# Kernel tuning notes

Hardware: AMD Instinct MI355X
Metric: run time of the kernel (lower is better)

The kernel has to match this reference:

```python
import jax, jax.numpy as jnp
import numpy as np

D_MODEL = 192; N_HEAD = 6; N_LEVELS = 3; N_POINTS = 4; D_HEAD = D_MODEL // N_HEAD
W_IMG = 1024.0; H_IMG = 1024.0
STRIDES = (8.0, 16.0, 32.0)
SIGMAS = (4.0, 2.0, 1.0)
N_FREQ = 8


def fourier_pe(coords):
    # coords [..., 2] -> [..., 4*N_FREQ]
    freqs = 2.0 ** jnp.arange(N_FREQ, dtype=jnp.float32)
    x = coords[..., 0:1] * freqs * (2.0 * jnp.pi)
    y = coords[..., 1:2] * freqs * (2.0 * jnp.pi)
    return jnp.concatenate([jnp.sin(x), jnp.cos(x), jnp.sin(y), jnp.cos(y)], axis=-1)


def bilinear_sample(feat, pts):
    # feat [B, H, d_h, Hl, Wl]; pts [B, K, R, H, M, 2] (x, y) in feature-pixel coords
    # zero padding outside the map (torch grid_sample padding_mode='zeros', align_corners=True)
    B, Hh, dh, Hl, Wl = feat.shape
    featf = feat.transpose(0, 1, 3, 4, 2).reshape(B, Hh, Hl * Wl, dh)
    x = pts[..., 0]; y = pts[..., 1]
    x0 = jnp.floor(x); y0 = jnp.floor(y)
    wx1 = x - x0; wy1 = y - y0
    wx0 = 1.0 - wx1; wy0 = 1.0 - wy1
    x0i = x0.astype(jnp.int32); y0i = y0.astype(jnp.int32)
    b_idx = jnp.arange(B)[:, None, None, None, None]
    h_idx = jnp.arange(Hh)[None, None, None, :, None]

    def gather(xi, yi):
        valid = (xi >= 0) & (xi < Wl) & (yi >= 0) & (yi < Hl)
        lin = jnp.clip(yi, 0, Hl - 1) * Wl + jnp.clip(xi, 0, Wl - 1)
        v = featf[b_idx, h_idx, lin]  # [B,K,R,H,M,dh]
        return v * valid[..., None].astype(feat.dtype)

    out = (gather(x0i, y0i) * (wx0 * wy0)[..., None]
           + gather(x0i + 1, y0i) * (wx1 * wy0)[..., None]
           + gather(x0i, y0i + 1) * (wx0 * wy1)[..., None]
           + gather(x0i + 1, y0i + 1) * (wx1 * wy1)[..., None])
    return out


def layernorm(x, g, b, eps=1e-5):
    mu = jnp.mean(x, axis=-1, keepdims=True)
    var = jnp.var(x, axis=-1, keepdims=True)
    return (x - mu) * jax.lax.rsqrt(var + eps) * g + b


def setup_inputs():
    key = jax.random.key(0)
    ks = jax.random.split(key, 16)
    B, K, R = 2, 256, 32
    H4 = W4 = 32
    s = 0.02
    inp = {}
    inp['h'] = jax.random.normal(ks[0], (B, K, D_MODEL), jnp.float32)
    inp['top_indices'] = jax.random.randint(ks[1], (B, K, R), 0, H4 * W4)
    inp['query_coords'] = jax.random.uniform(ks[2], (B, K, 2), jnp.float32) * jnp.array([W_IMG, H_IMG], jnp.float32)
    inp['g'] = jax.random.normal(ks[3], (B, H4 * W4, D_MODEL), jnp.float32)
    inp['L2_proj'] = jax.random.normal(ks[4], (B, D_MODEL, 128, 128), jnp.float32)
    inp['L3_proj'] = jax.random.normal(ks[5], (B, D_MODEL, 64, 64), jnp.float32)
    inp['L4_proj'] = jax.random.normal(ks[6], (B, D_MODEL, 32, 32), jnp.float32)
    inp['w_u_w'] = jax.random.normal(ks[7], (D_MODEL, 2 * D_MODEL + 32), jnp.float32) * s
    inp['w_u_b'] = jnp.zeros((D_MODEL,), jnp.float32)
    inp['ln_u_g'] = jnp.ones((D_MODEL,), jnp.float32)
    inp['ln_u_b'] = jnp.zeros((D_MODEL,), jnp.float32)
    inp['w_delta_w'] = jax.random.normal(ks[8], (N_HEAD * N_LEVELS * N_POINTS * 2, D_MODEL), jnp.float32) * s
    inp['w_delta_b'] = jax.random.normal(ks[9], (N_HEAD * N_LEVELS * N_POINTS * 2,), jnp.float32) * s
    inp['w_a_w'] = jax.random.normal(ks[10], (N_HEAD * N_LEVELS * N_POINTS, D_MODEL), jnp.float32) * s
    inp['w_a_b'] = jnp.zeros((N_HEAD * N_LEVELS * N_POINTS,), jnp.float32)
    inp['w_o_w'] = jax.random.normal(ks[11], (D_MODEL, D_MODEL), jnp.float32) * s
    inp['w_o_b'] = jnp.zeros((D_MODEL,), jnp.float32)
    inp['e_deform'] = jax.random.normal(ks[12], (1, 1, 1, D_MODEL), jnp.float32) * s
    return inp


def reference(h, top_indices, query_coords, g, L2_proj, L3_proj, L4_proj,
              w_u_w, w_u_b, ln_u_g, ln_u_b, w_delta_w, w_delta_b,
              w_a_w, w_a_b, w_o_w, w_o_b, e_deform):
    B, K, d = h.shape
    R = top_indices.shape[2]
    H, d_h, L, M = N_HEAD, D_HEAD, N_LEVELS, N_POINTS
    H4, W4 = L4_proj.shape[2], L4_proj.shape[3]

    # anchor pixel coordinates from L4 indices
    stride_4 = STRIDES[2]
    anchor_x = (top_indices % W4).astype(jnp.float32)
    anchor_y = (top_indices // W4).astype(jnp.float32)
    anchor_px = jnp.stack([anchor_x * stride_4 + stride_4 / 2,
                           anchor_y * stride_4 + stride_4 / 2], axis=-1)  # [B,K,R,2]

    # gather global tokens at anchors
    b_idx = jnp.arange(B)[:, None, None]
    g_r = g[b_idx, top_indices]  # [B,K,R,d]

    # relative position encoding
    delta_p = anchor_px - query_coords[:, :, None, :]
    delta_p_norm = delta_p / jnp.array([W_IMG, H_IMG], jnp.float32)
    phi = fourier_pe(delta_p_norm)  # [B,K,R,32]

    h_exp = jnp.broadcast_to(h[:, :, None, :], (B, K, R, d))
    u_input = jnp.concatenate([h_exp, g_r, phi], axis=-1)  # [B,K,R,2d+32]
    u_r = layernorm(jax.nn.gelu(jnp.einsum('bkrc,dc->bkrd', u_input, w_u_w) + w_u_b,
                                approximate=False), ln_u_g, ln_u_b)

    raw_offsets = (jnp.einsum('bkrd,od->bkro', u_r, w_delta_w) + w_delta_b
                   ).reshape(B, K, R, H, L, M, 2)
    logits = (jnp.einsum('bkrd,od->bkro', u_r, w_a_w) + w_a_b).reshape(B, K, R, H, L * M)
    weights = jax.nn.softmax(logits, axis=-1).reshape(B, K, R, H, L, M)

    proj_maps = [L2_proj, L3_proj, L4_proj]
    h_r = jnp.zeros((B, K, R, H, d_h), h.dtype)
    for l in range(L):
        feat = proj_maps[l]
        Hl, Wl = feat.shape[2], feat.shape[3]
        feat = feat.reshape(B, H, d_h, Hl, Wl)
        anchor_feat = anchor_px / STRIDES[l]  # [B,K,R,2]
        off = jnp.tanh(raw_offsets[:, :, :, :, l]) * SIGMAS[l]  # [B,K,R,H,M,2]
        pts = anchor_feat[:, :, :, None, None, :] + off  # [B,K,R,H,M,2]
        sampled = bilinear_sample(feat, pts)  # [B,K,R,H,M,d_h]
        h_r = h_r + jnp.einsum('bkrhmc,bkrhm->bkrhc', sampled, weights[:, :, :, :, l])

    h_r = h_r.reshape(B, K, R, d)
    deform_tokens = jnp.einsum('bkrd,od->bkro', h_r, w_o_w) + w_o_b + e_deform
    return deform_tokens
```

## Files before the change

### kernel.cpp

```cpp
#include <hip/hip_runtime.h>
#include <hip/hip_bf16.h>

typedef __hip_bfloat16 bf16;
typedef __attribute__((ext_vector_type(8))) short s8b;
typedef __attribute__((ext_vector_type(4))) float f32x4;

__device__ __forceinline__ float us2f(unsigned short u) {
  union { unsigned int i; float f; } v; v.i = ((unsigned int)u) << 16; return v.f;
}
__device__ __forceinline__ float ldf(const void* p, int i, bool f32m) {
  return f32m ? ((const float*)p)[i] : us2f(((const unsigned short*)p)[i]);
}
__device__ __forceinline__ bool sniff_f32(const void* ln_g_ones) {
  return ((const unsigned int*)ln_g_ones)[0] == 0x3F800000u;
}
__device__ __forceinline__ short f2bs(float x) {
  bf16 v = __float2bfloat16(x); short s; __builtin_memcpy(&s, &v, 2); return s;
}
__device__ __forceinline__ s8b cvt8(const float* p) {
  s8b r;
  #pragma unroll
  for (int j = 0; j < 8; ++j) r[j] = f2bs(p[j]);
  return r;
}

__global__ __launch_bounds__(256) void prep_all(
    const void* __restrict__ L2, const void* __restrict__ L3,
    const void* __restrict__ L4,
    const void* __restrict__ wu,  const void* __restrict__ wub,
    const void* __restrict__ lng, const void* __restrict__ lnb,
    const void* __restrict__ wd,  const void* __restrict__ wdb,
    const void* __restrict__ wa,  const void* __restrict__ wab,
    const void* __restrict__ wo,  const void* __restrict__ wob,
    const void* __restrict__ ed,  const void* __restrict__ h,
    bf16* __restrict__ f2, bf16* __restrict__ f3, bf16* __restrict__ f4,
    bf16* __restrict__ wb1, bf16* __restrict__ wb2, bf16* __restrict__ wb3,
    float* __restrict__ ln_g, float* __restrict__ ln_b,
    float* __restrict__ wda_b, float* __restrict__ wo_be,
    float* __restrict__ hdotAll, const int useT)
{
  __shared__ float tile[64][65];
  const bool f32m = sniff_f32(lng);
  const int t = threadIdx.x;
  int bid = blockIdx.x;

  if (bid < 2016) {
    if (!useT) return;
    const void* src; bf16* dst; int HW, spt;
    if (bid < 1536)      { src = L2; dst = f2; HW = 16384; spt = 256; }
    else if (bid < 1920) { bid -= 1536; src = L3; dst = f3; HW = 4096; spt = 64; }
    else                 { bid -= 1920; src = L4; dst = f4; HW = 1024; spt = 16; }
    int ct = bid % 3; bid /= 3;
    int st = bid % spt; int b = bid / spt;
    int sp0 = st * 64, ch0 = ct * 64;
    int sp4 = t & 15, cy0 = t >> 4;
    if (f32m) {
      #pragma unroll
      for (int i = 0; i < 4; ++i) {
        int cy = cy0 + 16 * i;
        const float* s4 = (const float*)src + (size_t)(b * 192 + ch0 + cy) * HW + sp0 + 4 * sp4;
        float4 v = *(const float4*)s4;
        tile[4 * sp4 + 0][cy] = v.x;
        tile[4 * sp4 + 1][cy] = v.y;
        tile[4 * sp4 + 2][cy] = v.z;
        tile[4 * sp4 + 3][cy] = v.w;
      }
    } else {
      #pragma unroll
      for (int i = 0; i < 4; ++i) {
        int cy = cy0 + 16 * i;
        #pragma unroll
        for (int k = 0; k < 4; ++k)
          tile[4 * sp4 + k][cy] =
              ldf(src, (b * 192 + ch0 + cy) * HW + sp0 + 4 * sp4 + k, f32m);
      }
    }
    __syncthreads();
    #pragma unroll
    for (int i = 0; i < 2; ++i) {
      int u = t + 256 * i;
      int sp = u >> 3, c8 = u & 7;
      const float* row = &tile[sp][c8 * 8];
      s8b pk;
      #pragma unroll
      for (int j = 0; j < 8; ++j) pk[j] = f2bs(row[j]);
      *(s8b*)&dst[(size_t)(b * HW + sp0 + sp) * 192 + ch0 + c8 * 8] = pk;
    }
  } else if (bid < 2528) {
    int i0 = (bid - 2016) * 256 + t;
    const int stride = 512 * 256;
    for (int i = i0; i < 192 * 224; i += stride) {
      int d = i / 224, cc = i - d * 224;
      int ks = cc >> 5, r32 = cc & 31, q = r32 >> 3, j = r32 & 7;
      int lane = q * 16 + (d & 15), nt = d >> 4;
      wb1[((ks * 12 + nt) * 64 + lane) * 8 + j] =
          __float2bfloat16(ldf(wu, d * 416 + 192 + cc, f32m));
    }
    for (int i = i0; i < 144 * 192; i += stride) {
      int o = i / 192, c = i - o * 192;
      int ks = c >> 5, r32 = c & 31, q = r32 >> 3, j = r32 & 7;
      int lane = q * 16 + (o & 15), nt = o >> 4;
      wb2[((ks * 14 + nt) * 64 + lane) * 8 + j] = __float2bfloat16(ldf(wd, i, f32m));
    }
    for (int i = i0; i < 72 * 192; i += stride) {
      int o = 144 + i / 192, c = i % 192;
      int ks = c >> 5, r32 = c & 31, q = r32 >> 3, j = r32 & 7;
      int lane = q * 16 + (o & 15), nt = o >> 4;
      wb2[((ks * 14 + nt) * 64 + lane) * 8 + j] = __float2bfloat16(ldf(wa, i, f32m));
    }
    for (int i = i0; i < 192 * 192; i += stride) {
      int o = i / 192, dK = i - o * 192;
      int ks = dK >> 5, r32 = dK & 31, q = r32 >> 3, j = r32 & 7;
      int lane = q * 16 + (o & 15), nt = o >> 4;
      wb3[((ks * 12 + nt) * 64 + lane) * 8 + j] = __float2bfloat16(ldf(wo, i, f32m));
    }
    if (i0 < 192) {
      ln_g[i0]  = ldf(lng, i0, f32m);
      ln_b[i0]  = ldf(lnb, i0, f32m);
      wo_be[i0] = ldf(wob, i0, f32m) + ldf(ed, i0, f32m);
    }
    if (i0 < 216) wda_b[i0] = (i0 < 144) ? ldf(wdb, i0, f32m) : ldf(wab, i0 - 144, f32m);
  } else {
    int bk = bid - 2528;
    int lane = t & 63, wv = t >> 6;
    float hv0 = ldf(h, bk * 192 + lane, f32m);
    float hv1 = ldf(h, bk * 192 + 64 + lane, f32m);
    float hv2 = ldf(h, bk * 192 + 128 + lane, f32m);
    for (int r = 0; r < 48; ++r) {
      int d = wv + 4 * r;
      float p = hv0 * ldf(wu, d * 416 + lane, f32m);
      p = fmaf(hv1, ldf(wu, d * 416 + 64 + lane, f32m), p);
      p = fmaf(hv2, ldf(wu, d * 416 + 128 + lane, f32m), p);
      #pragma unroll
      for (int off = 32; off >= 1; off >>= 1) p += __shfl_xor(p, off);
      if (lane == 0) hdotAll[bk * 192 + d] = p + ldf(wub, d, f32m);
    }
  }
}

__global__ __launch_bounds__(384) void fused_k(
    const int* __restrict__ topi, const void* __restrict__ qc,
    const void* __restrict__ g, const float* __restrict__ hdotAll,
    const bf16* __restrict__ wb1, const bf16* __restrict__ wb2,
    const bf16* __restrict__ wb3,
    const float* __restrict__ ln_g, const float* __restrict__ ln_b,
    const float* __restrict__ wda_b, const float* __restrict__ wo_be,
    const void* __restrict__ lng_raw,
    const bf16* __restrict__ f2, const bf16* __restrict__ f3,
    const bf16* __restrict__ f4,
    const void* __restrict__ L2, const void* __restrict__ L3,
    const void* __restrict__ L4, const int useT,
    float* __restrict__ out)
{
  __shared__ float uni[16 * 216];
  __shared__ float u_sh[16][196];
  __shared__ float anch[16][2];
  __shared__ int   idx_sh[16];
  __shared__ float qxy[2];
  __shared__ float stats[16][2];
  short* gpb = (short*)uni;
  float* ol  = uni;

  const bool f32m = sniff_f32(lng_raw);
  const int t = threadIdx.x;
  const int lane = t & 63, wv = t >> 6;
  const int m16 = lane & 15, quad = lane >> 4;
  const int bk = blockIdx.x >> 1;
  const int b = bk >> 8;
  const int tok0 = blockIdx.x * 16;

  if (t < 2) qxy[t] = ldf(qc, bk * 2 + t, f32m);
  if (t < 16) {
    int idx = topi[tok0 + t];
    idx_sh[t] = idx;
    anch[t][0] = (float)(idx & 31) * 32.f + 16.f;
    anch[t][1] = (float)(idx >> 5) * 32.f + 16.f;
  }
  __syncthreads();

  if (f32m) {
    #pragma unroll
    for (int i = 0; i < 2; ++i) {
      int u = t + 384 * i;
      int r = u / 48, q4 = u - r * 48;
      const float* s4 = (const float*)g + (size_t)(b * 1024 + idx_sh[r]) * 192 + 4 * q4;
      float4 v = *(const float4*)s4;
      short pk[4] = { f2bs(v.x), f2bs(v.y), f2bs(v.z), f2bs(v.w) };
      *(uint2*)&gpb[r * 232 + 4 * q4] = *(const uint2*)pk;
    }
  } else {
    for (int u = t; u < 16 * 192; u += 384) {
      int r = u / 192, j = u - r * 192;
      gpb[r * 232 + j] = f2bs(ldf(g, (b * 1024 + idx_sh[r]) * 192 + j, f32m));
    }
  }
  for (int u = t; u < 16 * 32; u += 384) {
    int r = u >> 5, j = u & 31;
    float dn = (((j & 16) ? (anch[r][1] - qxy[1]) : (anch[r][0] - qxy[0]))) * (1.f / 1024.f);
    float a = dn * (float)(1 << (j & 7)) * 6.283185307179586f;
    gpb[r * 232 + 192 + j] = f2bs((j & 8) ? cosf(a) : sinf(a));
  }
  __syncthreads();

  {
    s8b afr[7];
    #pragma unroll
    for (int ks = 0; ks < 7; ++ks)
      afr[ks] = *(const s8b*)&gpb[m16 * 232 + ks * 32 + quad * 8];
    const s8b* wbv = (const s8b*)wb1;
    #pragma unroll
    for (int nt = 0; nt < 2; ++nt) {
      int ntile = wv * 2 + nt;
      float bias = hdotAll[bk * 192 + ntile * 16 + m16];
      f32x4 acc = { bias, bias, bias, bias };
      #pragma unroll
      for (int ks = 0; ks < 7; ++ks) {
        s8b bfr = wbv[(ks * 12 + ntile) * 64 + lane];
        acc = __builtin_amdgcn_mfma_f32_16x16x32_bf16(afr[ks], bfr, acc, 0, 0, 0);
      }
      #pragma unroll
      for (int reg = 0; reg < 4; ++reg) {
        float x = acc[reg];
        u_sh[quad * 4 + reg][ntile * 16 + m16] =
            0.5f * x * (1.f + erff(x * 0.70710678118654752f));
      }
    }
  }
  __syncthreads();

  if (t < 256) {
    int r = t >> 4, i = t & 15;
    float s = 0.f, s2 = 0.f;
    #pragma unroll
    for (int j = 0; j < 12; ++j) { float v = u_sh[r][i * 12 + j]; s += v; s2 += v * v; }
    #pragma unroll
    for (int d = 8; d >= 1; d >>= 1) { s += __shfl_xor(s, d); s2 += __shfl_xor(s2, d); }
    if (i == 0) {
      float mu = s * (1.f / 192.f);
      float var = s2 * (1.f / 192.f) - mu * mu;
      stats[r][0] = mu; stats[r][1] = rsqrtf(var + 1e-5f);
    }
  }
  __syncthreads();
  for (int u = t; u < 16 * 192; u += 384) {
    int r = u / 192, dd = u - r * 192;
    u_sh[r][dd] = (u_sh[r][dd] - stats[r][0]) * stats[r][1] * ln_g[dd] + ln_b[dd];
  }
  __syncthreads();

  {
    s8b afr[6];
    #pragma unroll
    for (int ks = 0; ks < 6; ++ks)
      afr[ks] = cvt8(&u_sh[m16][ks * 32 + quad * 8]);
    const s8b* wbv = (const s8b*)wb2;
    #pragma unroll
    for (int i = 0; i < 3; ++i) {
      int ntile = wv + 6 * i;
      if (ntile < 14) {
        int o0 = ntile * 16 + m16;
        float bias = (o0 < 216) ? wda_b[o0] : 0.f;
        f32x4 acc = { bias, bias, bias, bias };
        #pragma unroll
        for (int ks = 0; ks < 6; ++ks) {
          s8b bfr = wbv[(ks * 14 + ntile) * 64 + lane];
          acc = __builtin_amdgcn_mfma_f32_16x16x32_bf16(afr[ks], bfr, acc, 0, 0, 0);
        }
        if (o0 < 216) {
          #pragma unroll
          for (int reg = 0; reg < 4; ++reg)
            ol[(quad * 4 + reg) * 216 + o0] = acc[reg];
        }
      }
    }
  }
  __syncthreads();

  for (int u = t; u < 16 * 144; u += 384) {
    int r = u / 144, o = u - r * 144;
    int l = (o >> 3) % 3;
    ol[r * 216 + o] = tanhf(ol[r * 216 + o]) * (float)(4 >> l);
  }
  if (t < 96) {
    int r = t / 6, hh = t - r * 6;
    float* lg = &ol[r * 216 + 144 + hh * 12];
    float mx = lg[0];
    for (int i = 1; i < 12; ++i) mx = fmaxf(mx, lg[i]);
    float s = 0.f;
    for (int i = 0; i < 12; ++i) { float e = expf(lg[i] - mx); lg[i] = e; s += e; }
    float inv = 1.f / s;
    for (int i = 0; i < 12; ++i) lg[i] *= inv;
  }
  __syncthreads();

  {
    int tl = t / 24, c8 = t - tl * 24;
    int hc0 = c8 * 8;
    int hh = hc0 >> 5;
    float ax = anch[tl][0], ay = anch[tl][1];
    const float* olp = &ol[tl * 216];
    float acc[8];
    #pragma unroll
    for (int j = 0; j < 8; ++j) acc[j] = 0.f;

    const bf16* ftsT[3] = { f2, f3, f4 };
    const void* ftsO[3] = { L2, L3, L4 };
    #pragma unroll
    for (int l = 0; l < 3; ++l) {
      const int Hl = 128 >> l;
      const bf16* ftT = ftsT[l];
      const void* ftO = ftsO[l];
      float inv_s = 1.f / (float)(8 << l);
      float bx = ax * inv_s, by = ay * inv_s;
      #pragma unroll
      for (int m = 0; m < 4; ++m) {
        int ob = ((hh * 3 + l) * 4 + m) * 2;
        float px = bx + olp[ob];
        float py = by + olp[ob + 1];
        float fx = floorf(px), fy = floorf(py);
        int x0 = (int)fx, y0 = (int)fy;
        float wx1 = px - fx, wy1 = py - fy;
        float wx0 = 1.f - wx1, wy0 = 1.f - wy1;
        int xc0 = min(max(x0, 0), Hl - 1),   xc1 = min(max(x0 + 1, 0), Hl - 1);
        int yc0 = min(max(y0, 0), Hl - 1),   yc1 = min(max(y0 + 1, 0), Hl - 1);
        bool vx0 = (x0 >= 0) & (x0 < Hl),    vx1 = (x0 + 1 >= 0) & (x0 + 1 < Hl);
        bool vy0 = (y0 >= 0) & (y0 < Hl),    vy1 = (y0 + 1 >= 0) & (y0 + 1 < Hl);
        float aw = olp[144 + hh * 12 + l * 4 + m];
        float w00 = (vx0 && vy0) ? wx0 * wy0 * aw : 0.f;
        float w01 = (vx1 && vy0) ? wx1 * wy0 * aw : 0.f;
        float w10 = (vx0 && vy1) ? wx0 * wy1 * aw : 0.f;
        float w11 = (vx1 && vy1) ? wx1 * wy1 * aw : 0.f;
        if (useT) {
          const s8b* p00 = (const s8b*)&ftT[((b * Hl + yc0) * Hl + xc0) * 192 + hc0];
          const s8b* p01 = (const s8b*)&ftT[((b * Hl + yc0) * Hl + xc1) * 192 + hc0];
          const s8b* p10 = (const s8b*)&ftT[((b * Hl + yc1) * Hl + xc0) * 192 + hc0];
          const s8b* p11 = (const s8b*)&ftT[((b * Hl + yc1) * Hl + xc1) * 192 + hc0];
          s8b v00 = *p00, v01 = *p01, v10 = *p10, v11 = *p11;
          #pragma unroll
          for (int j = 0; j < 8; ++j) {
            float s = us2f((unsigned short)v00[j]) * w00
                    + us2f((unsigned short)v01[j]) * w01
                    + us2f((unsigned short)v10[j]) * w10
                    + us2f((unsigned short)v11[j]) * w11;
            acc[j] += s;
          }
        } else {
          #pragma unroll
          for (int j = 0; j < 8; ++j) {
            int ch = hc0 + j;
            float s = ldf(ftO, ((b * 192 + ch) * Hl + yc0) * Hl + xc0, f32m) * w00
                    + ldf(ftO, ((b * 192 + ch) * Hl + yc0) * Hl + xc1, f32m) * w01
                    + ldf(ftO, ((b * 192 + ch) * Hl + yc1) * Hl + xc0, f32m) * w10
                    + ldf(ftO, ((b * 192 + ch) * Hl + yc1) * Hl + xc1, f32m) * w11;
            acc[j] += s;
          }
        }
      }
    }
    #pragma unroll
    for (int j = 0; j < 8; ++j) u_sh[tl][hc0 + j] = acc[j];
  }
  __syncthreads();

  {
    s8b afr[6];
    #pragma unroll
    for (int ks = 0; ks < 6; ++ks)
      afr[ks] = cvt8(&u_sh[m16][ks * 32 + quad * 8]);
    const s8b* wbv = (const s8b*)wb3;
    #pragma unroll
    for (int nt = 0; nt < 2; ++nt) {
      int ntile = wv * 2 + nt;
      int n = ntile * 16 + m16;
      float bias = wo_be[n];
      f32x4 acc = { bias, bias, bias, bias };
      #pragma unroll
      for (int ks = 0; ks < 6; ++ks) {
        s8b bfr = wbv[(ks * 12 + ntile) * 64 + lane];
        acc = __builtin_amdgcn_mfma_f32_16x16x32_bf16(afr[ks], bfr, acc, 0, 0, 0);
      }
      #pragma unroll
      for (int reg = 0; reg < 4; ++reg)
        out[(long long)(tok0 + quad * 4 + reg) * 192 + n] = acc[reg];
    }
  }
}

extern "C" void kernel_launch(void* const* d_in, const int* in_sizes, int n_in,
                              void* d_out, int out_size, void* d_ws, size_t ws_size,
                              hipStream_t stream)
{
  const void* h    = d_in[0];
  const int*  topi = (const int*)d_in[1];
  const void* qc   = d_in[2];
  const void* g    = d_in[3];
  const void* L2p  = d_in[4];
  const void* L3p  = d_in[5];
  const void* L4p  = d_in[6];
  const void* wu   = d_in[7];
  const void* wub  = d_in[8];
  const void* lng  = d_in[9];
  const void* lnb  = d_in[10];
  const void* wd   = d_in[11];
  const void* wdb  = d_in[12];
  const void* wa   = d_in[13];
  const void* wab  = d_in[14];
  const void* wo   = d_in[15];
  const void* wob  = d_in[16];
  const void* ed   = d_in[17];
  float* outp = (float*)d_out;

  char* ws = (char*)d_ws;
  size_t off = 0;
  auto take = [&](size_t bytes) {
    char* p = ws + off;
    off += (bytes + 255) & ~(size_t)255;
    return p;
  };
  bf16*  wb1     = (bf16*)take(7ULL * 12 * 64 * 8 * 2);
  bf16*  wb2     = (bf16*)take(6ULL * 14 * 64 * 8 * 2);
  bf16*  wb3     = (bf16*)take(6ULL * 12 * 64 * 8 * 2);
  float* lngf    = (float*)take(192 * 4);
  float* lnbf    = (float*)take(192 * 4);
  float* wda_b   = (float*)take(216 * 4);
  float* wo_be   = (float*)take(192 * 4);
  float* hdotAll = (float*)take(512ULL * 192 * 4);
  size_t feat_bytes = (2ULL * 192 * 128 * 128 + 2ULL * 192 * 64 * 64 + 2ULL * 192 * 32 * 32) * 2 + 1024;
  int useT = (ws_size >= off + feat_bytes) ? 1 : 0;
  bf16* f2 = (bf16*)take(useT ? 2ULL * 192 * 128 * 128 * 2 : 0);
  bf16* f3 = (bf16*)take(useT ? 2ULL * 192 * 64 * 64 * 2 : 0);
  bf16* f4 = (bf16*)take(useT ? 2ULL * 192 * 32 * 32 * 2 : 0);
  (void)in_sizes; (void)n_in; (void)out_size;

  hipLaunchKernelGGL(prep_all, dim3(3040), dim3(256), 0, stream,
                     L2p, L3p, L4p, wu, wub, lng, lnb, wd, wdb, wa, wab,
                     wo, wob, ed, h, f2, f3, f4, wb1, wb2, wb3,
                     lngf, lnbf, wda_b, wo_be, hdotAll, useT);
  hipLaunchKernelGGL(fused_k, dim3(1024), dim3(384), 0, stream,
                     topi, qc, g, hdotAll, wb1, wb2, wb3,
                     lngf, lnbf, wda_b, wo_be, lng,
                     f2, f3, f4, L2p, L3p, L4p, useT, outp);
}
```

Before: 192.2 us.

## Replace LDS-tiled feature transpose with direct per-thread gather and packed bf16 FMA

The feature-map NCHW→NHWC bf16 conversion in the prep kernel drops its 64x64 shared-memory tile transpose. Each thread now reads 8 channel values directly with strided loads and writes one 16-byte packed vector, and the grid grows to match. The sampling loop in the fused kernel also unpacks bf16 pairs from 32-bit words and accumulates into 2-wide float vectors, to allow packed FMA. The direct gather gives up coalesced reads in the transpose, since the 8 loads per thread hit addresses HW apart, which may raise global memory traffic in exchange for removing the LDS round trip and the barrier.

```diff
diff --git a/kernel.cpp b/kernel.cpp
--- a/kernel.cpp
+++ b/kernel.cpp
@@ -4,6 +4,7 @@
 typedef __hip_bfloat16 bf16;
 typedef __attribute__((ext_vector_type(8))) short s8b;
 typedef __attribute__((ext_vector_type(4))) float f32x4;
+typedef __attribute__((ext_vector_type(2))) float v2f;
 
 __device__ __forceinline__ float us2f(unsigned short u) {
   union { unsigned int i; float f; } v; v.i = ((unsigned int)u) << 16; return v.f;
@@ -22,6 +23,11 @@
   #pragma unroll
   for (int j = 0; j < 8; ++j) r[j] = f2bs(p[j]);
   return r;
+}
+__device__ __forceinline__ v2f bf2x(unsigned int u) {
+  union { unsigned int i; float f; } lo, hi;
+  lo.i = u << 16; hi.i = u & 0xffff0000u;
+  v2f r; r.x = lo.f; r.y = hi.f; return r;
 }
 
 __global__ __launch_bounds__(256) void prep_all(
@@ -39,55 +45,25 @@
     float* __restrict__ wda_b, float* __restrict__ wo_be,
     float* __restrict__ hdotAll, const int useT)
 {
-  __shared__ float tile[64][65];
   const bool f32m = sniff_f32(lng);
   const int t = threadIdx.x;
   int bid = blockIdx.x;
 
-  if (bid < 2016) {
+  if (bid < 4032) {
     if (!useT) return;
-    const void* src; bf16* dst; int HW, spt;
-    if (bid < 1536)      { src = L2; dst = f2; HW = 16384; spt = 256; }
-    else if (bid < 1920) { bid -= 1536; src = L3; dst = f3; HW = 4096; spt = 64; }
-    else                 { bid -= 1920; src = L4; dst = f4; HW = 1024; spt = 16; }
-    int ct = bid % 3; bid /= 3;
-    int st = bid % spt; int b = bid / spt;
-    int sp0 = st * 64, ch0 = ct * 64;
-    int sp4 = t & 15, cy0 = t >> 4;
-    if (f32m) {
-      #pragma unroll
-      for (int i = 0; i < 4; ++i) {
-        int cy = cy0 + 16 * i;
-        const float* s4 = (const float*)src + (size_t)(b * 192 + ch0 + cy) * HW + sp0 + 4 * sp4;
-        float4 v = *(const float4*)s4;
-        tile[4 * sp4 + 0][cy] = v.x;
-        tile[4 * sp4 + 1][cy] = v.y;
-        tile[4 * sp4 + 2][cy] = v.z;
-        tile[4 * sp4 + 3][cy] = v.w;
-      }
-    } else {
-      #pragma unroll
-      for (int i = 0; i < 4; ++i) {
-        int cy = cy0 + 16 * i;
-        #pragma unroll
-        for (int k = 0; k < 4; ++k)
-          tile[4 * sp4 + k][cy] =
-              ldf(src, (b * 192 + ch0 + cy) * HW + sp0 + 4 * sp4 + k, f32m);
-      }
-    }
-    __syncthreads();
-    #pragma unroll
-    for (int i = 0; i < 2; ++i) {
-      int u = t + 256 * i;
-      int sp = u >> 3, c8 = u & 7;
-      const float* row = &tile[sp][c8 * 8];
-      s8b pk;
-      #pragma unroll
-      for (int j = 0; j < 8; ++j) pk[j] = f2bs(row[j]);
-      *(s8b*)&dst[(size_t)(b * HW + sp0 + sp) * 192 + ch0 + c8 * 8] = pk;
-    }
-  } else if (bid < 2528) {
-    int i0 = (bid - 2016) * 256 + t;
+    int u = bid * 256 + t;
+    int c8 = u % 24, gpix = u / 24;
+    const void* src; bf16* dst; int HW, b, sp;
+    if (gpix < 32768)      { src = L2; dst = f2; HW = 16384; b = gpix >> 14; sp = gpix & 16383; }
+    else if (gpix < 40960) { gpix -= 32768; src = L3; dst = f3; HW = 4096; b = gpix >> 12; sp = gpix & 4095; }
+    else                   { gpix -= 40960; src = L4; dst = f4; HW = 1024; b = gpix >> 10; sp = gpix & 1023; }
+    s8b pk;
+    #pragma unroll
+    for (int j = 0; j < 8; ++j)
+      pk[j] = f2bs(ldf(src, (b * 192 + c8 * 8 + j) * HW + sp, f32m));
+    *(s8b*)&dst[(size_t)(b * HW + sp) * 192 + c8 * 8] = pk;
+  } else if (bid < 4544) {
+    int i0 = (bid - 4032) * 256 + t;
     const int stride = 512 * 256;
     for (int i = i0; i < 192 * 224; i += stride) {
       int d = i / 224, cc = i - d * 224;
@@ -121,7 +97,7 @@
     }
     if (i0 < 216) wda_b[i0] = (i0 < 144) ? ldf(wdb, i0, f32m) : ldf(wab, i0 - 144, f32m);
   } else {
-    int bk = bid - 2528;
+    int bk = bid - 4544;
     int lane = t & 63, wv = t >> 6;
     float hv0 = ldf(h, bk * 192 + lane, f32m);
     float hv1 = ldf(h, bk * 192 + 64 + lane, f32m);
@@ -299,9 +275,9 @@
     int hh = hc0 >> 5;
     float ax = anch[tl][0], ay = anch[tl][1];
     const float* olp = &ol[tl * 216];
-    float acc[8];
-    #pragma unroll
-    for (int j = 0; j < 8; ++j) acc[j] = 0.f;
+    v2f acc2[4];
+    #pragma unroll
+    for (int p = 0; p < 4; ++p) { acc2[p].x = 0.f; acc2[p].y = 0.f; }
 
     const bf16* ftsT[3] = { f2, f3, f4 };
     const void* ftsO[3] = { L2, L3, L4 };
@@ -331,34 +307,42 @@
         float w10 = (vx0 && vy1) ? wx0 * wy1 * aw : 0.f;
         float w11 = (vx1 && vy1) ? wx1 * wy1 * aw : 0.f;
         if (useT) {
-          const s8b* p00 = (const s8b*)&ftT[((b * Hl + yc0) * Hl + xc0) * 192 + hc0];
-          const s8b* p01 = (const s8b*)&ftT[((b * Hl + yc0) * Hl + xc1) * 192 + hc0];
-          const s8b* p10 = (const s8b*)&ftT[((b * Hl + yc1) * Hl + xc0) * 192 + hc0];
-          const s8b* p11 = (const s8b*)&ftT[((b * Hl + yc1) * Hl + xc1) * 192 + hc0];
-          s8b v00 = *p00, v01 = *p01, v10 = *p10, v11 = *p11;
+          uint4 u00 = *(const uint4*)&ftT[((b * Hl + yc0) * Hl + xc0) * 192 + hc0];
+          uint4 u01 = *(const uint4*)&ftT[((b * Hl + yc0) * Hl + xc1) * 192 + hc0];
+          uint4 u10 = *(const uint4*)&ftT[((b * Hl + yc1) * Hl + xc0) * 192 + hc0];
+          uint4 u11 = *(const uint4*)&ftT[((b * Hl + yc1) * Hl + xc1) * 192 + hc0];
+          const unsigned int* a0 = (const unsigned int*)&u00;
+          const unsigned int* a1 = (const unsigned int*)&u01;
+          const unsigned int* a2 = (const unsigned int*)&u10;
+          const unsigned int* a3 = (const unsigned int*)&u11;
           #pragma unroll
-          for (int j = 0; j < 8; ++j) {
-            float s = us2f((unsigned short)v00[j]) * w00
-                    + us2f((unsigned short)v01[j]) * w01
-                    + us2f((unsigned short)v10[j]) * w10
-                    + us2f((unsigned short)v11[j]) * w11;
-            acc[j] += s;
+          for (int p = 0; p < 4; ++p) {
+            acc2[p] += bf2x(a0[p]) * w00;
+            acc2[p] += bf2x(a1[p]) * w01;
+            acc2[p] += bf2x(a2[p]) * w10;
+            acc2[p] += bf2x(a3[p]) * w11;
           }
         } else {
           #pragma unroll
-          for (int j = 0; j < 8; ++j) {
-            int ch = hc0 + j;
-            float s = ldf(ftO, ((b * 192 + ch) * Hl + yc0) * Hl + xc0, f32m) * w00
-                    + ldf(ftO, ((b * 192 + ch) * Hl + yc0) * Hl + xc1, f32m) * w01
-                    + ldf(ftO, ((b * 192 + ch) * Hl + yc1) * Hl + xc0, f32m) * w10
-                    + ldf(ftO, ((b * 192 + ch) * Hl + yc1) * Hl + xc1, f32m) * w11;
-            acc[j] += s;
+          for (int p = 0; p < 4; ++p) {
+            #pragma unroll
+            for (int e = 0; e < 2; ++e) {
+              int ch = hc0 + 2 * p + e;
+              float s = ldf(ftO, ((b * 192 + ch) * Hl + yc0) * Hl + xc0, f32m) * w00
+                      + ldf(ftO, ((b * 192 + ch) * Hl + yc0) * Hl + xc1, f32m) * w01
+                      + ldf(ftO, ((b * 192 + ch) * Hl + yc1) * Hl + xc0, f32m) * w10
+                      + ldf(ftO, ((b * 192 + ch) * Hl + yc1) * Hl + xc1, f32m) * w11;
+              if (e == 0) acc2[p].x += s; else acc2[p].y += s;
+            }
           }
         }
       }
     }
     #pragma unroll
-    for (int j = 0; j < 8; ++j) u_sh[tl][hc0 + j] = acc[j];
+    for (int p = 0; p < 4; ++p) {
+      u_sh[tl][hc0 + 2 * p]     = acc2[p].x;
+      u_sh[tl][hc0 + 2 * p + 1] = acc2[p].y;
+    }
   }
   __syncthreads();
 
@@ -432,7 +416,7 @@
   bf16* f4 = (bf16*)take(useT ? 2ULL * 192 * 32 * 32 * 2 : 0);
   (void)in_sizes; (void)n_in; (void)out_size;
 
-  hipLaunchKernelGGL(prep_all, dim3(3040), dim3(256), 0, stream,
+  hipLaunchKernelGGL(prep_all, dim3(5056), dim3(256), 0, stream,
                      L2p, L3p, L4p, wu, wub, lng, lnb, wd, wdb, wa, wab,
                      wo, wob, ed, h, f2, f3, f4, wb1, wb2, wb3,
                      lngf, lnbf, wda_b, wo_be, hdotAll, useT);
```

New measurement: 194.3 us. Within noise of the previous version (+1.1%).
